# Optimization experiments

Measured on AMD Instinct MI355X. Metric: run time of the kernel, lower is better.

The kernel has to match this reference:

```python
import jax, jax.numpy as jnp
import numpy as np

B, S, H, I, E, TOP_K = 2, 2048, 1024, 2048, 8, 2


def setup_inputs() -> dict:
    key = jax.random.key(0)
    k1, k2, k3, k4, k5 = jax.random.split(key, 5)
    scale_h = 1.0 / np.sqrt(H)
    scale_i = 1.0 / np.sqrt(I)
    return {
        "hidden_states": jax.random.normal(k1, (B, S, H), dtype=jnp.float32),
        "router_w": jax.random.normal(k2, (H, E), dtype=jnp.float32) * scale_h,
        "gate_w": jax.random.normal(k3, (E, H, I), dtype=jnp.float32) * scale_h,
        "up_w": jax.random.normal(k4, (E, H, I), dtype=jnp.float32) * scale_h,
        "out_w": jax.random.normal(k5, (E, I, H), dtype=jnp.float32) * scale_i,
    }


def reference(hidden_states, router_w, gate_w, up_w, out_w):
    b, s, h = hidden_states.shape
    x = hidden_states.reshape(-1, h)  # [T, H], T = B*S

    # Router: logits -> softmax -> top-k -> renormalize -> dense routing matrix
    router_logits = x @ router_w  # [T, E]
    router_probs = jax.nn.softmax(router_logits, axis=-1)
    top_p, top_i = jax.lax.top_k(router_probs, TOP_K)  # [T, K]
    top_p = top_p / jnp.sum(top_p, axis=-1, keepdims=True)
    one_hot = jax.nn.one_hot(top_i, E, dtype=top_p.dtype)  # [T, K, E]
    routing_full = jnp.sum(one_hot * top_p[..., None], axis=1)  # [T, E]
    routing_full = routing_full.T  # [E, T]

    # Dense all-expert FFN (SwiGLU), as in the original batched einsum form
    gate = jnp.einsum("th,ehm->etm", x, gate_w)  # [E, T, I]
    gate = jax.nn.silu(gate)
    intermediate = jnp.einsum("th,ehm->etm", x, up_w)  # [E, T, I]
    hidden = intermediate * gate
    expert_out = jnp.einsum("eti,eih->eth", hidden, out_w)  # [E, T, H]

    # Weighted combine over experts
    out = jnp.sum(expert_out * routing_full[:, :, None], axis=0)  # [T, H]
    out = out.reshape(b, s, h)
    return out, router_logits
```

## Files before the change

### kernel.cpp

```cpp
#include <hip/hip_runtime.h>
#include <hip/hip_bf16.h>
#include <stdint.h>

#define TT 4096
#define HH 1024
#define II 2048
#define EE 8
#define RB 16
#define NRB (TT / RB)
#define CSTRIDE 32

typedef short bf16x8 __attribute__((ext_vector_type(8)));
typedef float f32x4 __attribute__((ext_vector_type(4)));

__device__ __forceinline__ unsigned short f2bf(float f) {
  unsigned u = __float_as_uint(f);
  u += 0x7FFF + ((u >> 16) & 1);
  return (unsigned short)(u >> 16);
}

__device__ __forceinline__ void gl_lds16(const void* g, void* l) {
  auto gp = reinterpret_cast<const __attribute__((address_space(1))) unsigned int*>(
      reinterpret_cast<uintptr_t>(g));
  auto lp = reinterpret_cast<__attribute__((address_space(3))) unsigned int*>(
      reinterpret_cast<uintptr_t>(l));
  __builtin_amdgcn_global_load_lds(gp, lp, 16, 0, 0);
}

__device__ __forceinline__ void transpose_tile_wide(const float* __restrict__ in,
                                                    unsigned short* __restrict__ out,
                                                    int M, int N, int mB, int nB,
                                                    unsigned int* tl, int tid) {
  union F4 { float4 v; float f[4]; };
  int n4 = tid & 31;
  int mph = tid >> 5;
  F4 a[4], bq[4];
  const float* base = in + (size_t)mB * N + nB + n4 * 4;
#pragma unroll
  for (int it = 0; it < 4; ++it) {
    const float* p = base + (size_t)(2 * (mph + it * 8)) * N;
    a[it].v = *(const float4*)p;
    bq[it].v = *(const float4*)(p + N);
  }
#pragma unroll
  for (int it = 0; it < 4; ++it) {
    int mp = mph + it * 8;
#pragma unroll
    for (int i = 0; i < 4; ++i) {
      int n = n4 * 4 + i;
      unsigned v = (unsigned)f2bf(a[it].f[i]) | ((unsigned)f2bf(bq[it].f[i]) << 16);
      tl[n * 32 + ((mp + (n >> 2) + (n & 3)) & 31)] = v;
    }
  }
  __syncthreads();
  int md = tid & 7;
  int nr = tid >> 3;
#pragma unroll
  for (int it = 0; it < 4; ++it) {
    int n = nr + it * 32;
    int rot = (n >> 2) + (n & 3);
    unsigned vv[4];
#pragma unroll
    for (int k = 0; k < 4; ++k)
      vv[k] = tl[n * 32 + ((md * 4 + k + rot) & 31)];
    *(uint4*)(out + (size_t)(nB + n) * M + mB + md * 8) = make_uint4(vv[0], vv[1], vv[2], vv[3]);
  }
}

__global__ __launch_bounds__(256, 4)
void front_kernel(const float* __restrict__ x, const float* __restrict__ rw,
                  const float* __restrict__ gw, const float* __restrict__ uw,
                  const float* __restrict__ ow,
                  float* __restrict__ logits_out, unsigned short* __restrict__ xb,
                  unsigned short* __restrict__ gwt, unsigned short* __restrict__ uwt,
                  unsigned short* __restrict__ owt,
                  int* __restrict__ gcnt, int2* __restrict__ ttop) {
  __shared__ unsigned int tl[4096];
  int b = blockIdx.x;
  int tid = threadIdx.x;

  if (b >= NRB) {
    int idx = b - NRB;
    int which = idx >> 11;
    int r = idx & 2047;
    int e = r >> 8;
    int tile = r & 255;
    if (which < 2) {
      int bx = tile & 15, by = tile >> 4;
      const float* in = (which ? uw : gw) + (size_t)e * HH * II;
      unsigned short* o = (which ? uwt : gwt) + (size_t)e * HH * II;
      transpose_tile_wide(in, o, HH, II, by * 64, bx * 128, tl, tid);
    } else {
      int bx = tile & 7, by = tile >> 3;
      transpose_tile_wide(ow + (size_t)e * II * HH, owt + (size_t)e * II * HH,
                          II, HH, by * 64, bx * 128, tl, tid);
    }
    return;
  }

  __shared__ int bcnt[EE];
  int wave = tid >> 6, lane = tid & 63;
  if (tid < EE) bcnt[tid] = 0;
  __syncthreads();
  int t0 = b * RB;

  for (int sub = 0; sub < RB / 4; ++sub) {
    int li = sub * 4 + wave;
    int t = t0 + li;
    float acc[EE];
#pragma unroll
    for (int e = 0; e < EE; ++e) acc[e] = 0.f;
#pragma unroll
    for (int j = 0; j < 4; ++j) {
      int h = j * 256 + lane * 4;
      union F4 { float4 v; float f[4]; } xv;
      xv.v = *(const float4*)(x + (size_t)t * HH + h);
      union { unsigned short s[4]; uint2 v; } pk;
#pragma unroll
      for (int i = 0; i < 4; ++i) pk.s[i] = f2bf(xv.f[i]);
      *(uint2*)(xb + (size_t)t * HH + h) = pk.v;
#pragma unroll
      for (int i = 0; i < 4; ++i) {
        const float4* r4 = (const float4*)(rw + (h + i) * EE);
        float4 r0 = r4[0], r1 = r4[1];
        float xs = xv.f[i];
        acc[0] += xs * r0.x; acc[1] += xs * r0.y; acc[2] += xs * r0.z; acc[3] += xs * r0.w;
        acc[4] += xs * r1.x; acc[5] += xs * r1.y; acc[6] += xs * r1.z; acc[7] += xs * r1.w;
      }
    }
#pragma unroll
    for (int e = 0; e < EE; ++e)
#pragma unroll
      for (int off = 32; off; off >>= 1) acc[e] += __shfl_down(acc[e], off);
    if (lane == 0) {
      float4* lo = (float4*)(logits_out + (size_t)t * EE);
      lo[0] = make_float4(acc[0], acc[1], acc[2], acc[3]);
      lo[1] = make_float4(acc[4], acc[5], acc[6], acc[7]);
      int e0 = 0; float b0 = acc[0];
#pragma unroll
      for (int e = 1; e < EE; ++e) if (acc[e] > b0) { b0 = acc[e]; e0 = e; }
      int e1 = -1; float b1 = -3.4e38f;
#pragma unroll
      for (int e = 0; e < EE; ++e) if (e != e0 && acc[e] > b1) { b1 = acc[e]; e1 = e; }
      float w0 = 1.f / (1.f + __expf(b1 - b0));
      int lp0 = atomicAdd(&bcnt[e0], 1);
      int lp1 = atomicAdd(&bcnt[e1], 1);
      ttop[t] = make_int2(e0 | (e1 << 3) | (lp0 << 6) | (lp1 << 11), __float_as_int(w0));
    }
  }
  __syncthreads();
  if (tid < EE) gcnt[b * EE + tid] = bcnt[tid];
}

__global__ void scatter_kernel(const int* __restrict__ gcnt, const int2* __restrict__ ttop,
                               int* __restrict__ cnt, int* __restrict__ list,
                               int* __restrict__ tslot, float2* __restrict__ tw) {
  __shared__ int raw[NRB * EE];
  __shared__ int base[NRB][EE];
  int tid = threadIdx.x;
  for (int i = tid; i < NRB * EE; i += 256) raw[i] = gcnt[i];
  __syncthreads();
  if (tid < EE) {
    int s = 0;
    for (int b = 0; b < NRB; ++b) { base[b][tid] = s; s += raw[b * EE + tid]; }
    if (blockIdx.x == 0) cnt[tid * CSTRIDE] = s;
  }
  __syncthreads();
  int t = blockIdx.x * 256 + tid;
  int2 ti = ttop[t];
  int v = ti.x;
  float w0 = __int_as_float(ti.y);
  int e0 = v & 7, e1 = (v >> 3) & 7, lp0 = (v >> 6) & 31, lp1 = (v >> 11) & 31;
  int b = t >> 4;
  int p0 = base[b][e0] + lp0;
  int p1 = base[b][e1] + lp1;
  list[e0 * TT + p0] = t;
  list[e1 * TT + p1] = t;
  tslot[t * 2]     = (e0 << 16) | p0;
  tslot[t * 2 + 1] = (e1 << 16) | p1;
  tw[t] = make_float2(w0, 1.f - w0);
}

__launch_bounds__(256, 3)
__global__ void gemm1_kernel(const unsigned short* __restrict__ xb,
                             const unsigned short* __restrict__ gwt,
                             const unsigned short* __restrict__ uwt,
                             unsigned short* __restrict__ hidden,
                             const int* __restrict__ cnt, const int* __restrict__ list) {
  __shared__ __align__(16) unsigned short smem[16384];
  __shared__ int stok[128];
  int tid = threadIdx.x;
  int e = blockIdx.z;

  int cn = cnt[e * CSTRIDE];
  int hb0 = 0;
  for (int i = 0; i < EE; ++i) hb0 += (i < e) ? cnt[i * CSTRIDE] : 0;
  int mBase = blockIdx.y * 128;
  if (mBase >= cn) return;
  int nBase = blockIdx.x * 64;

  int wave = tid >> 6, lane = tid & 63;
  if (tid < 128) {
    int g = mBase + tid;
    stok[tid] = list[e * TT + (g < cn ? g : cn - 1)];
  }
  __syncthreads();

  const char* gaddr[8];
#pragma unroll
  for (int j = 0; j < 8; ++j) {
    int c = wave * 512 + j * 64 + lane;
    const char* g;
    if (c < 1024) {
      int r = c >> 3, sl = (c & 7) ^ (r & 7);
      g = (const char*)xb + (size_t)stok[r] * (HH * 2) + sl * 16;
    } else if (c < 1536) {
      int cc = c - 1024, r = cc >> 3, sl = (cc & 7) ^ (r & 7);
      g = (const char*)gwt + ((size_t)e * II + nBase + r) * (HH * 2) + sl * 16;
    } else {
      int cc = c - 1536, r = cc >> 3, sl = (cc & 7) ^ (r & 7);
      g = (const char*)uwt + ((size_t)e * II + nBase + r) * (HH * 2) + sl * 16;
    }
    gaddr[j] = g;
  }

  int q = lane >> 4, m16 = lane & 15;
  int wr = wave & 1, wc = wave >> 1;
  int faddrA[4][2], faddrBg[2][2], faddrBu[2][2];
#pragma unroll
  for (int mi = 0; mi < 4; ++mi) {
    int R = wr * 64 + mi * 16 + m16;
#pragma unroll
    for (int h = 0; h < 2; ++h)
      faddrA[mi][h] = (R * 8 + ((h * 4 + q) ^ (R & 7))) * 16;
  }
#pragma unroll
  for (int ni = 0; ni < 2; ++ni) {
    int n = wc * 32 + ni * 16 + m16;
#pragma unroll
    for (int h = 0; h < 2; ++h) {
      faddrBg[ni][h] = (1024 + n * 8 + ((h * 4 + q) ^ (n & 7))) * 16;
      faddrBu[ni][h] = (1536 + n * 8 + ((h * 4 + q) ^ (n & 7))) * 16;
    }
  }

  f32x4 zero4 = {0.f, 0.f, 0.f, 0.f};
  f32x4 accG[4][2], accU[4][2];
#pragma unroll
  for (int mi = 0; mi < 4; ++mi)
#pragma unroll
    for (int ni = 0; ni < 2; ++ni) { accG[mi][ni] = zero4; accU[mi][ni] = zero4; }

  const char* smemc = (const char*)smem;
  for (int kt = 0; kt < HH / 64; ++kt) {
    __syncthreads();
#pragma unroll
    for (int j = 0; j < 8; ++j) {
      gl_lds16(gaddr[j], (char*)smem + (size_t)(wave * 512 + j * 64) * 16);
      gaddr[j] += 128;
    }
    __syncthreads();
#pragma unroll
    for (int h = 0; h < 2; ++h) {
      bf16x8 aF[4], bG[2], bU[2];
#pragma unroll
      for (int mi = 0; mi < 4; ++mi) aF[mi] = *(const bf16x8*)(smemc + faddrA[mi][h]);
#pragma unroll
      for (int ni = 0; ni < 2; ++ni) {
        bG[ni] = *(const bf16x8*)(smemc + faddrBg[ni][h]);
        bU[ni] = *(const bf16x8*)(smemc + faddrBu[ni][h]);
      }
#pragma unroll
      for (int mi = 0; mi < 4; ++mi)
#pragma unroll
        for (int ni = 0; ni < 2; ++ni) {
          accG[mi][ni] = __builtin_amdgcn_mfma_f32_16x16x32_bf16(aF[mi], bG[ni], accG[mi][ni], 0, 0, 0);
          accU[mi][ni] = __builtin_amdgcn_mfma_f32_16x16x32_bf16(aF[mi], bU[ni], accU[mi][ni], 0, 0, 0);
        }
    }
  }

  int hb = hb0 + mBase;
  int rowsValid = cn - mBase; if (rowsValid > 128) rowsValid = 128;
#pragma unroll
  for (int mi = 0; mi < 4; ++mi)
#pragma unroll
    for (int ni = 0; ni < 2; ++ni)
#pragma unroll
      for (int r = 0; r < 4; ++r) {
        int row = wr * 64 + mi * 16 + q * 4 + r;
        if (row < rowsValid) {
          float g = accG[mi][ni][r], u = accU[mi][ni][r];
          float h = g / (1.f + __expf(-g)) * u;
          hidden[(size_t)(hb + row) * II + nBase + wc * 32 + ni * 16 + m16] = f2bf(h);
        }
      }
}

__launch_bounds__(256, 3)
__global__ void gemm2_kernel(const unsigned short* __restrict__ hidden,
                             const unsigned short* __restrict__ owt,
                             float* __restrict__ expert_out,
                             const int* __restrict__ cnt) {
  int e = blockIdx.z;
  int cn = cnt[e * CSTRIDE];
  int hb0 = 0;
  for (int i = 0; i < EE; ++i) hb0 += (i < e) ? cnt[i * CSTRIDE] : 0;
  int mBase = blockIdx.y * 128;
  if (mBase >= cn) return;
  int nBase = blockIdx.x * 128;

  __shared__ __align__(16) unsigned short smem[16384];

  int tid = threadIdx.x, wave = tid >> 6, lane = tid & 63;
  int hb = hb0 + mBase;
  const char* gaddr[8];
#pragma unroll
  for (int j = 0; j < 8; ++j) {
    int c = wave * 512 + j * 64 + lane;
    const char* g;
    if (c < 1024) {
      int r = c >> 3, sl = (c & 7) ^ (r & 7);
      g = (const char*)hidden + (size_t)(hb + r) * (II * 2) + sl * 16;
    } else {
      int cc = c - 1024, r = cc >> 3, sl = (cc & 7) ^ (r & 7);
      g = (const char*)owt + ((size_t)e * HH + nBase + r) * (II * 2) + sl * 16;
    }
    gaddr[j] = g;
  }

  int q = lane >> 4, m16 = lane & 15;
  int wr = wave & 1, wc = wave >> 1;
  int faddrA[4][2], faddrB[4][2];
#pragma unroll
  for (int mi = 0; mi < 4; ++mi) {
    int R = wr * 64 + mi * 16 + m16;
#pragma unroll
    for (int h = 0; h < 2; ++h)
      faddrA[mi][h] = (R * 8 + ((h * 4 + q) ^ (R & 7))) * 16;
  }
#pragma unroll
  for (int ni = 0; ni < 4; ++ni) {
    int n = wc * 64 + ni * 16 + m16;
#pragma unroll
    for (int h = 0; h < 2; ++h)
      faddrB[ni][h] = (1024 + n * 8 + ((h * 4 + q) ^ (n & 7))) * 16;
  }

  f32x4 zero4 = {0.f, 0.f, 0.f, 0.f};
  f32x4 acc[4][4];
#pragma unroll
  for (int mi = 0; mi < 4; ++mi)
#pragma unroll
    for (int ni = 0; ni < 4; ++ni) acc[mi][ni] = zero4;

  const char* smemc = (const char*)smem;
  for (int kt = 0; kt < II / 64; ++kt) {
    __syncthreads();
#pragma unroll
    for (int j = 0; j < 8; ++j) {
      gl_lds16(gaddr[j], (char*)smem + (size_t)(wave * 512 + j * 64) * 16);
      gaddr[j] += 128;
    }
    __syncthreads();
#pragma unroll
    for (int h = 0; h < 2; ++h) {
      bf16x8 aF[4], bF[4];
#pragma unroll
      for (int mi = 0; mi < 4; ++mi) aF[mi] = *(const bf16x8*)(smemc + faddrA[mi][h]);
#pragma unroll
      for (int ni = 0; ni < 4; ++ni) bF[ni] = *(const bf16x8*)(smemc + faddrB[ni][h]);
#pragma unroll
      for (int mi = 0; mi < 4; ++mi)
#pragma unroll
        for (int ni = 0; ni < 4; ++ni)
          acc[mi][ni] = __builtin_amdgcn_mfma_f32_16x16x32_bf16(aF[mi], bF[ni], acc[mi][ni], 0, 0, 0);
    }
  }

  int rowsValid = cn - mBase; if (rowsValid > 128) rowsValid = 128;
#pragma unroll
  for (int mi = 0; mi < 4; ++mi)
#pragma unroll
    for (int ni = 0; ni < 4; ++ni)
#pragma unroll
      for (int r = 0; r < 4; ++r) {
        int row = wr * 64 + mi * 16 + q * 4 + r;
        if (row < rowsValid)
          expert_out[(size_t)(hb + row) * HH + nBase + wc * 64 + ni * 16 + m16] = acc[mi][ni][r];
      }
}

__global__ void combine_kernel(const float* __restrict__ expert_out,
                               const int* __restrict__ cnt, const int* __restrict__ tslot,
                               const float2* __restrict__ tw, float* __restrict__ out) {
  int pre[EE];
  int s = 0;
#pragma unroll
  for (int e = 0; e < EE; ++e) { pre[e] = s; s += cnt[e * CSTRIDE]; }
  int t = blockIdx.x;
  int s0 = tslot[t * 2], s1 = tslot[t * 2 + 1];
  float2 w = tw[t];
  int r0 = pre[s0 >> 16] + (s0 & 0xFFFF);
  int r1 = pre[s1 >> 16] + (s1 & 0xFFFF);
  const float4* a = (const float4*)(expert_out + (size_t)r0 * HH);
  const float4* b = (const float4*)(expert_out + (size_t)r1 * HH);
  float4* o = (float4*)(out + (size_t)t * HH);
  int c = threadIdx.x;
  float4 av = a[c], bv = b[c];
  o[c] = make_float4(w.x * av.x + w.y * bv.x, w.x * av.y + w.y * bv.y,
                     w.x * av.z + w.y * bv.z, w.x * av.w + w.y * bv.w);
}

extern "C" void kernel_launch(void* const* d_in, const int* in_sizes, int n_in,
                              void* d_out, int out_size, void* d_ws, size_t ws_size,
                              hipStream_t stream) {
  (void)in_sizes; (void)n_in; (void)out_size; (void)ws_size;
  const float* x  = (const float*)d_in[0];
  const float* rw = (const float*)d_in[1];
  const float* gw = (const float*)d_in[2];
  const float* uw = (const float*)d_in[3];
  const float* ow = (const float*)d_in[4];
  float* out = (float*)d_out;
  float* logits = out + (size_t)TT * HH;

  char* ws = (char*)d_ws;
  size_t o = 0;
  auto alloc = [&](size_t bytes) {
    char* p = ws + o;
    o += (bytes + 255) & ~(size_t)255;
    return p;
  };
  unsigned short* xb  = (unsigned short*)alloc((size_t)TT * HH * 2);
  unsigned short* gwt = (unsigned short*)alloc((size_t)EE * II * HH * 2);
  unsigned short* uwt = (unsigned short*)alloc((size_t)EE * II * HH * 2);
  unsigned short* owt = (unsigned short*)alloc((size_t)EE * HH * II * 2);
  unsigned short* hidden = (unsigned short*)alloc((size_t)(2 * TT + 128) * II * 2);
  int*    cnt   = (int*)alloc(EE * CSTRIDE * 4);
  int*    list  = (int*)alloc((size_t)EE * TT * 4);
  int*    tslot = (int*)alloc((size_t)TT * 2 * 4);
  float2* tw    = (float2*)alloc((size_t)TT * 8);
  int*    gcnt  = (int*)alloc((size_t)NRB * EE * 4);
  int2*   ttop  = (int2*)alloc((size_t)TT * 8);
  float* expert_out = (float*)gwt;

  front_kernel<<<NRB + 3 * 2048, 256, 0, stream>>>(x, rw, gw, uw, ow, logits, xb, gwt, uwt, owt,
                                                   gcnt, ttop);
  scatter_kernel<<<TT / 256, 256, 0, stream>>>(gcnt, ttop, cnt, list, tslot, tw);
  gemm1_kernel<<<dim3(32, 32, EE), 256, 0, stream>>>(xb, gwt, uwt, hidden, cnt, list);
  gemm2_kernel<<<dim3(HH / 128, TT / 128, EE), 256, 0, stream>>>(hidden, owt, expert_out, cnt);
  combine_kernel<<<TT, 256, 0, stream>>>(expert_out, cnt, tslot, tw, out);
}
```

Measured before the change: 398.9 us.

## Process four transpose tiles per block with double-buffered register prefetch

The weight transpose/convert path now handles four consecutive 64x128 tiles per block instead of one. The global loads for the next tile are issued into a second register set while the current tile is converted and written through an LDS buffer, alternating between two LDS buffers. The aim is to hide global load latency and amortize per-block launch overhead across tiles. In exchange, register use per thread and LDS per block both double, which may reduce occupancy in the shared front_kernel, including its router blocks.

After: 406.8 us. No clear change (+2.0%).

```diff
diff --git a/kernel.cpp b/kernel.cpp
--- a/kernel.cpp
+++ b/kernel.cpp
@@ -27,43 +27,56 @@
   __builtin_amdgcn_global_load_lds(gp, lp, 16, 0, 0);
 }
 
-__device__ __forceinline__ void transpose_tile_wide(const float* __restrict__ in,
-                                                    unsigned short* __restrict__ out,
-                                                    int M, int N, int mB, int nB,
-                                                    unsigned int* tl, int tid) {
+__device__ __forceinline__ void transpose_quad(const float* __restrict__ in,
+                                               unsigned short* __restrict__ out,
+                                               int M, int N, int mB, int bx0,
+                                               unsigned int* tl, int tid) {
   union F4 { float4 v; float f[4]; };
   int n4 = tid & 31;
   int mph = tid >> 5;
-  F4 a[4], bq[4];
-  const float* base = in + (size_t)mB * N + nB + n4 * 4;
-#pragma unroll
-  for (int it = 0; it < 4; ++it) {
-    const float* p = base + (size_t)(2 * (mph + it * 8)) * N;
-    a[it].v = *(const float4*)p;
-    bq[it].v = *(const float4*)(p + N);
-  }
-#pragma unroll
-  for (int it = 0; it < 4; ++it) {
-    int mp = mph + it * 8;
-#pragma unroll
-    for (int i = 0; i < 4; ++i) {
-      int n = n4 * 4 + i;
-      unsigned v = (unsigned)f2bf(a[it].f[i]) | ((unsigned)f2bf(bq[it].f[i]) << 16);
-      tl[n * 32 + ((mp + (n >> 2) + (n & 3)) & 31)] = v;
-    }
-  }
-  __syncthreads();
-  int md = tid & 7;
-  int nr = tid >> 3;
-#pragma unroll
-  for (int it = 0; it < 4; ++it) {
-    int n = nr + it * 32;
-    int rot = (n >> 2) + (n & 3);
-    unsigned vv[4];
-#pragma unroll
-    for (int k = 0; k < 4; ++k)
-      vv[k] = tl[n * 32 + ((md * 4 + k + rot) & 31)];
-    *(uint4*)(out + (size_t)(nB + n) * M + mB + md * 8) = make_uint4(vv[0], vv[1], vv[2], vv[3]);
+  F4 R0[8], R1[8];
+
+  auto issue = [&](F4* R, int nB) {
+    const float* base = in + (size_t)(mB + 2 * mph) * N + nB + n4 * 4;
+#pragma unroll
+    for (int it = 0; it < 4; ++it) {
+      const float* p = base + (size_t)(2 * it * 8) * N;
+      R[it].v = *(const float4*)p;
+      R[4 + it].v = *(const float4*)(p + N);
+    }
+  };
+
+  issue(R0, bx0 * 128);
+#pragma unroll
+  for (int i = 0; i < 4; ++i) {
+    F4* cur = (i & 1) ? R1 : R0;
+    F4* nxt = (i & 1) ? R0 : R1;
+    if (i < 3) issue(nxt, (bx0 + i + 1) * 128);
+    unsigned int* buf = tl + (i & 1) * 4096;
+    int nB = (bx0 + i) * 128;
+#pragma unroll
+    for (int it = 0; it < 4; ++it) {
+      int mp = mph + it * 8;
+#pragma unroll
+      for (int k = 0; k < 4; ++k) {
+        int n = n4 * 4 + k;
+        unsigned v = (unsigned)f2bf(cur[it].f[k]) | ((unsigned)f2bf(cur[4 + it].f[k]) << 16);
+        buf[n * 32 + ((mp + (n >> 2) + (n & 3)) & 31)] = v;
+      }
+    }
+    __syncthreads();
+    int md = tid & 7;
+    int nr = tid >> 3;
+#pragma unroll
+    for (int it = 0; it < 4; ++it) {
+      int n = nr + it * 32;
+      int rot = (n >> 2) + (n & 3);
+      unsigned vv[4];
+#pragma unroll
+      for (int k = 0; k < 4; ++k)
+        vv[k] = buf[n * 32 + ((md * 4 + k + rot) & 31)];
+      *(uint4*)(out + (size_t)(nB + n) * M + mB + md * 8) = make_uint4(vv[0], vv[1], vv[2], vv[3]);
+    }
   }
 }
 
@@ -75,25 +88,25 @@
                   unsigned short* __restrict__ gwt, unsigned short* __restrict__ uwt,
                   unsigned short* __restrict__ owt,
                   int* __restrict__ gcnt, int2* __restrict__ ttop) {
-  __shared__ unsigned int tl[4096];
+  __shared__ unsigned int tl[8192];
   int b = blockIdx.x;
   int tid = threadIdx.x;
 
   if (b >= NRB) {
     int idx = b - NRB;
-    int which = idx >> 11;
-    int r = idx & 2047;
-    int e = r >> 8;
-    int tile = r & 255;
+    int which = idx >> 9;
+    int r = idx & 511;
+    int e = r >> 6;
+    int blk = r & 63;
     if (which < 2) {
-      int bx = tile & 15, by = tile >> 4;
+      int mB = (blk >> 2) * 64, bx0 = (blk & 3) * 4;
       const float* in = (which ? uw : gw) + (size_t)e * HH * II;
       unsigned short* o = (which ? uwt : gwt) + (size_t)e * HH * II;
-      transpose_tile_wide(in, o, HH, II, by * 64, bx * 128, tl, tid);
+      transpose_quad(in, o, HH, II, mB, bx0, tl, tid);
     } else {
-      int bx = tile & 7, by = tile >> 3;
-      transpose_tile_wide(ow + (size_t)e * II * HH, owt + (size_t)e * II * HH,
-                          II, HH, by * 64, bx * 128, tl, tid);
+      int mB = (blk >> 1) * 64, bx0 = (blk & 1) * 4;
+      transpose_quad(ow + (size_t)e * II * HH, owt + (size_t)e * II * HH,
+                     II, HH, mB, bx0, tl, tid);
     }
     return;
   }
@@ -444,8 +457,8 @@
   int2*   ttop  = (int2*)alloc((size_t)TT * 8);
   float* expert_out = (float*)gwt;
 
-  front_kernel<<<NRB + 3 * 2048, 256, 0, stream>>>(x, rw, gw, uw, ow, logits, xb, gwt, uwt, owt,
-                                                   gcnt, ttop);
+  front_kernel<<<NRB + 3 * 512, 256, 0, stream>>>(x, rw, gw, uw, ow, logits, xb, gwt, uwt, owt,
+                                                  gcnt, ttop);
   scatter_kernel<<<TT / 256, 256, 0, stream>>>(gcnt, ttop, cnt, list, tslot, tw);
   gemm1_kernel<<<dim3(32, 32, EE), 256, 0, stream>>>(xb, gwt, uwt, hidden, cnt, list);
   gemm2_kernel<<<dim3(HH / 128, TT / 128, EE), 256, 0, stream>>>(hidden, owt, expert_out, cnt);
```

## Double-buffer LDS tiles with K=32 steps in both expert GEMMs

Applied to the files above, without the earlier changes.

Both expert GEMM kernels now split their 32KB of LDS into two 16KB buffers with a K-tile of 32 instead of one 32KB buffer with a K-tile of 64. The direct global-to-LDS loads for the next tile are issued before the MFMA work on the current tile, leaving one barrier per iteration. The aim is to hide global load latency behind matrix math instead of stalling on a load-then-compute barrier pair. To match the new 4-chunk row width, the XOR swizzle changes to (row>>1)&3. Each tile now feeds half as many MFMAs, so per-iteration overhead is relatively larger.

After: 419.3 us. +5.1%, slower.

```diff
diff --git a/kernel.cpp b/kernel.cpp
--- a/kernel.cpp
+++ b/kernel.cpp
@@ -206,42 +206,39 @@
   }
   __syncthreads();
 
-  const char* gaddr[8];
-#pragma unroll
-  for (int j = 0; j < 8; ++j) {
-    int c = wave * 512 + j * 64 + lane;
+  const char* gaddr[4];
+  int lofs[4];
+#pragma unroll
+  for (int j = 0; j < 4; ++j) {
+    int c = wave * 256 + j * 64 + lane;
     const char* g;
-    if (c < 1024) {
-      int r = c >> 3, sl = (c & 7) ^ (r & 7);
-      g = (const char*)xb + (size_t)stok[r] * (HH * 2) + sl * 16;
-    } else if (c < 1536) {
-      int cc = c - 1024, r = cc >> 3, sl = (cc & 7) ^ (r & 7);
-      g = (const char*)gwt + ((size_t)e * II + nBase + r) * (HH * 2) + sl * 16;
+    if (c < 512) {
+      int r = c >> 2, kc = (c & 3) ^ ((r >> 1) & 3);
+      g = (const char*)xb + (size_t)stok[r] * (HH * 2) + kc * 16;
+    } else if (c < 768) {
+      int cc = c - 512, r = cc >> 2, kc = (cc & 3) ^ ((r >> 1) & 3);
+      g = (const char*)gwt + ((size_t)e * II + nBase + r) * (HH * 2) + kc * 16;
     } else {
-      int cc = c - 1536, r = cc >> 3, sl = (cc & 7) ^ (r & 7);
-      g = (const char*)uwt + ((size_t)e * II + nBase + r) * (HH * 2) + sl * 16;
+      int cc = c - 768, r = cc >> 2, kc = (cc & 3) ^ ((r >> 1) & 3);
+      g = (const char*)uwt + ((size_t)e * II + nBase + r) * (HH * 2) + kc * 16;
     }
     gaddr[j] = g;
+    lofs[j] = c * 16;
   }
 
   int q = lane >> 4, m16 = lane & 15;
   int wr = wave & 1, wc = wave >> 1;
-  int faddrA[4][2], faddrBg[2][2], faddrBu[2][2];
+  int faddrA[4], faddrBg[2], faddrBu[2];
 #pragma unroll
   for (int mi = 0; mi < 4; ++mi) {
     int R = wr * 64 + mi * 16 + m16;
-#pragma unroll
-    for (int h = 0; h < 2; ++h)
-      faddrA[mi][h] = (R * 8 + ((h * 4 + q) ^ (R & 7))) * 16;
+    faddrA[mi] = (R * 4 + (q ^ ((R >> 1) & 3))) * 16;
   }
 #pragma unroll
   for (int ni = 0; ni < 2; ++ni) {
     int n = wc * 32 + ni * 16 + m16;
-#pragma unroll
-    for (int h = 0; h < 2; ++h) {
-      faddrBg[ni][h] = (1024 + n * 8 + ((h * 4 + q) ^ (n & 7))) * 16;
-      faddrBu[ni][h] = (1536 + n * 8 + ((h * 4 + q) ^ (n & 7))) * 16;
-    }
+    faddrBg[ni] = (512 + n * 4 + (q ^ ((n >> 1) & 3))) * 16;
+    faddrBu[ni] = (768 + n * 4 + (q ^ ((n >> 1) & 3))) * 16;
   }
 
   f32x4 zero4 = {0.f, 0.f, 0.f, 0.f};
@@ -251,33 +248,41 @@
 #pragma unroll
     for (int ni = 0; ni < 2; ++ni) { accG[mi][ni] = zero4; accU[mi][ni] = zero4; }
 
-  const char* smemc = (const char*)smem;
-  for (int kt = 0; kt < HH / 64; ++kt) {
+  char* smemc = (char*)smem;
+#pragma unroll
+  for (int j = 0; j < 4; ++j) {
+    gl_lds16(gaddr[j], smemc + lofs[j]);
+    gaddr[j] += 64;
+  }
+  __syncthreads();
+
+  const int NK = HH / 32;
+  for (int kt = 0; kt < NK; ++kt) {
+    int cur = kt & 1;
+    if (kt + 1 < NK) {
+#pragma unroll
+      for (int j = 0; j < 4; ++j) {
+        gl_lds16(gaddr[j], smemc + (cur ^ 1) * 16384 + lofs[j]);
+        gaddr[j] += 64;
+      }
+    }
+    const char* sb = smemc + cur * 16384;
+    bf16x8 aF[4], bG[2], bU[2];
+#pragma unroll
+    for (int mi = 0; mi < 4; ++mi) aF[mi] = *(const bf16x8*)(sb + faddrA[mi]);
+#pragma unroll
+    for (int ni = 0; ni < 2; ++ni) {
+      bG[ni] = *(const bf16x8*)(sb + faddrBg[ni]);
+      bU[ni] = *(const bf16x8*)(sb + faddrBu[ni]);
+    }
+#pragma unroll
+    for (int mi = 0; mi < 4; ++mi)
+#pragma unroll
+      for (int ni = 0; ni < 2; ++ni) {
+        accG[mi][ni] = __builtin_amdgcn_mfma_f32_16x16x32_bf16(aF[mi], bG[ni], accG[mi][ni], 0, 0, 0);
+        accU[mi][ni] = __builtin_amdgcn_mfma_f32_16x16x32_bf16(aF[mi], bU[ni], accU[mi][ni], 0, 0, 0);
+      }
     __syncthreads();
-#pragma unroll
-    for (int j = 0; j < 8; ++j) {
-      gl_lds16(gaddr[j], (char*)smem + (size_t)(wave * 512 + j * 64) * 16);
-      gaddr[j] += 128;
-    }
-    __syncthreads();
-#pragma unroll
-    for (int h = 0; h < 2; ++h) {
-      bf16x8 aF[4], bG[2], bU[2];
-#pragma unroll
-      for (int mi = 0; mi < 4; ++mi) aF[mi] = *(const bf16x8*)(smemc + faddrA[mi][h]);
-#pragma unroll
-      for (int ni = 0; ni < 2; ++ni) {
-        bG[ni] = *(const bf16x8*)(smemc + faddrBg[ni][h]);
-        bU[ni] = *(const bf16x8*)(smemc + faddrBu[ni][h]);
-      }
-#pragma unroll
-      for (int mi = 0; mi < 4; ++mi)
-#pragma unroll
-        for (int ni = 0; ni < 2; ++ni) {
-          accG[mi][ni] = __builtin_amdgcn_mfma_f32_16x16x32_bf16(aF[mi], bG[ni], accG[mi][ni], 0, 0, 0);
-          accU[mi][ni] = __builtin_amdgcn_mfma_f32_16x16x32_bf16(aF[mi], bU[ni], accU[mi][ni], 0, 0, 0);
-        }
-    }
   }
 
   int hb = hb0 + mBase;
@@ -314,37 +319,35 @@
 
   int tid = threadIdx.x, wave = tid >> 6, lane = tid & 63;
   int hb = hb0 + mBase;
-  const char* gaddr[8];
-#pragma unroll
-  for (int j = 0; j < 8; ++j) {
-    int c = wave * 512 + j * 64 + lane;
+  const char* gaddr[4];
+  int lofs[4];
+#pragma unroll
+  for (int j = 0; j < 4; ++j) {
+    int c = wave * 256 + j * 64 + lane;
     const char* g;
-    if (c < 1024) {
-      int r = c >> 3, sl = (c & 7) ^ (r & 7);
-      g = (const char*)hidden + (size_t)(hb + r) * (II * 2) + sl * 16;
+    if (c < 512) {
+      int r = c >> 2, kc = (c & 3) ^ ((r >> 1) & 3);
+      g = (const char*)hidden + (size_t)(hb + r) * (II * 2) + kc * 16;
     } else {
-      int cc = c - 1024, r = cc >> 3, sl = (cc & 7) ^ (r & 7);
-      g = (const char*)owt + ((size_t)e * HH + nBase + r) * (II * 2) + sl * 16;
+      int cc = c - 512, r = cc >> 2, kc = (cc & 3) ^ ((r >> 1) & 3);
+      g = (const char*)owt + ((size_t)e * HH + nBase + r) * (II * 2) + kc * 16;
     }
     gaddr[j] = g;
+    lofs[j] = c * 16;
   }
 
   int q = lane >> 4, m16 = lane & 15;
   int wr = wave & 1, wc = wave >> 1;
-  int faddrA[4][2], faddrB[4][2];
+  int faddrA[4], faddrB[4];
 #pragma unroll
   for (int mi = 0; mi < 4; ++mi) {
     int R = wr * 64 + mi * 16 + m16;
-#pragma unroll
-    for (int h = 0; h < 2; ++h)
-      faddrA[mi][h] = (R * 8 + ((h * 4 + q) ^ (R & 7))) * 16;
+    faddrA[mi] = (R * 4 + (q ^ ((R >> 1) & 3))) * 16;
   }
 #pragma unroll
   for (int ni = 0; ni < 4; ++ni) {
     int n = wc * 64 + ni * 16 + m16;
-#pragma unroll
-    for (int h = 0; h < 2; ++h)
-      faddrB[ni][h] = (1024 + n * 8 + ((h * 4 + q) ^ (n & 7))) * 16;
+    faddrB[ni] = (512 + n * 4 + (q ^ ((n >> 1) & 3))) * 16;
   }
 
   f32x4 zero4 = {0.f, 0.f, 0.f, 0.f};
@@ -354,28 +357,36 @@
 #pragma unroll
     for (int ni = 0; ni < 4; ++ni) acc[mi][ni] = zero4;
 
-  const char* smemc = (const char*)smem;
-  for (int kt = 0; kt < II / 64; ++kt) {
+  char* smemc = (char*)smem;
+#pragma unroll
+  for (int j = 0; j < 4; ++j) {
+    gl_lds16(gaddr[j], smemc + lofs[j]);
+    gaddr[j] += 64;
+  }
+  __syncthreads();
+
+  const int NK = II / 32;
+  for (int kt = 0; kt < NK; ++kt) {
+    int cur = kt & 1;
+    if (kt + 1 < NK) {
+#pragma unroll
+      for (int j = 0; j < 4; ++j) {
+        gl_lds16(gaddr[j], smemc + (cur ^ 1) * 16384 + lofs[j]);
+        gaddr[j] += 64;
+      }
+    }
+    const char* sb = smemc + cur * 16384;
+    bf16x8 aF[4], bF[4];
+#pragma unroll
+    for (int mi = 0; mi < 4; ++mi) aF[mi] = *(const bf16x8*)(sb + faddrA[mi]);
+#pragma unroll
+    for (int ni = 0; ni < 4; ++ni) bF[ni] = *(const bf16x8*)(sb + faddrB[ni]);
+#pragma unroll
+    for (int mi = 0; mi < 4; ++mi)
+#pragma unroll
+      for (int ni = 0; ni < 4; ++ni)
+        acc[mi][ni] = __builtin_amdgcn_mfma_f32_16x16x32_bf16(aF[mi], bF[ni], acc[mi][ni], 0, 0, 0);
     __syncthreads();
-#pragma unroll
-    for (int j = 0; j < 8; ++j) {
-      gl_lds16(gaddr[j], (char*)smem + (size_t)(wave * 512 + j * 64) * 16);
-      gaddr[j] += 128;
-    }
-    __syncthreads();
-#pragma unroll
-    for (int h = 0; h < 2; ++h) {
-      bf16x8 aF[4], bF[4];
-#pragma unroll
-      for (int mi = 0; mi < 4; ++mi) aF[mi] = *(const bf16x8*)(smemc + faddrA[mi][h]);
-#pragma unroll
-      for (int ni = 0; ni < 4; ++ni) bF[ni] = *(const bf16x8*)(smemc + faddrB[ni][h]);
-#pragma unroll
-      for (int mi = 0; mi < 4; ++mi)
-#pragma unroll
-        for (int ni = 0; ni < 4; ++ni)
-          acc[mi][ni] = __builtin_amdgcn_mfma_f32_16x16x32_bf16(aF[mi], bF[ni], acc[mi][ni], 0, 0, 0);
-    }
   }
 
   int rowsValid = cn - mBase; if (rowsValid > 128) rowsValid = 128;
```

## Fuse weighted combine into gemm2 via atomics and move out_w transpose into gemm1

Applied to the files above, without the earlier changes.

Drops the separate combine kernel and the fp32 expert_out buffer. gemm2 now scales each output row by its routing weight and atomically adds it into the zero-initialised output, and the output is zeroed by extra blocks in the front kernel. The out_w transpose moves from the front kernel into extra blocks of gemm1, so it can overlap with the first GEMM. The cost is float atomics on global memory, which make the summation order nondeterministic, and more blocks in the gemm1 launch.

After: 398.3 us. Within noise of the previous version (-0.1%).

```diff
diff --git a/kernel.cpp b/kernel.cpp
--- a/kernel.cpp
+++ b/kernel.cpp
@@ -9,6 +9,8 @@
 #define RB 16
 #define NRB (TT / RB)
 #define CSTRIDE 32
+#define NTRB (2 * 2048)
+#define NZB 256
 
 typedef short bf16x8 __attribute__((ext_vector_type(8)));
 typedef float f32x4 __attribute__((ext_vector_type(4)));
@@ -70,14 +72,22 @@
 __global__ __launch_bounds__(256, 4)
 void front_kernel(const float* __restrict__ x, const float* __restrict__ rw,
                   const float* __restrict__ gw, const float* __restrict__ uw,
-                  const float* __restrict__ ow,
                   float* __restrict__ logits_out, unsigned short* __restrict__ xb,
                   unsigned short* __restrict__ gwt, unsigned short* __restrict__ uwt,
-                  unsigned short* __restrict__ owt,
-                  int* __restrict__ gcnt, int2* __restrict__ ttop) {
+                  int* __restrict__ gcnt, int2* __restrict__ ttop,
+                  float* __restrict__ outz) {
   __shared__ unsigned int tl[4096];
   int b = blockIdx.x;
   int tid = threadIdx.x;
+
+  if (b >= NRB + NTRB) {
+    int zb = b - NRB - NTRB;
+    float4* o = (float4*)outz + (size_t)zb * 4096 + tid;
+    float4 z = make_float4(0.f, 0.f, 0.f, 0.f);
+#pragma unroll
+    for (int k = 0; k < 16; ++k) o[k * 256] = z;
+    return;
+  }
 
   if (b >= NRB) {
     int idx = b - NRB;
@@ -85,16 +95,10 @@
     int r = idx & 2047;
     int e = r >> 8;
     int tile = r & 255;
-    if (which < 2) {
-      int bx = tile & 15, by = tile >> 4;
-      const float* in = (which ? uw : gw) + (size_t)e * HH * II;
-      unsigned short* o = (which ? uwt : gwt) + (size_t)e * HH * II;
-      transpose_tile_wide(in, o, HH, II, by * 64, bx * 128, tl, tid);
-    } else {
-      int bx = tile & 7, by = tile >> 3;
-      transpose_tile_wide(ow + (size_t)e * II * HH, owt + (size_t)e * II * HH,
-                          II, HH, by * 64, bx * 128, tl, tid);
-    }
+    int bx = tile & 15, by = tile >> 4;
+    const float* in = (which ? uw : gw) + (size_t)e * HH * II;
+    unsigned short* o = (which ? uwt : gwt) + (size_t)e * HH * II;
+    transpose_tile_wide(in, o, HH, II, by * 64, bx * 128, tl, tid);
     return;
   }
 
@@ -154,7 +158,7 @@
 
 __global__ void scatter_kernel(const int* __restrict__ gcnt, const int2* __restrict__ ttop,
                                int* __restrict__ cnt, int* __restrict__ list,
-                               int* __restrict__ tslot, float2* __restrict__ tw) {
+                               float* __restrict__ rwt) {
   __shared__ int raw[NRB * EE];
   __shared__ int base[NRB][EE];
   int tid = threadIdx.x;
@@ -176,21 +180,29 @@
   int p1 = base[b][e1] + lp1;
   list[e0 * TT + p0] = t;
   list[e1 * TT + p1] = t;
-  tslot[t * 2]     = (e0 << 16) | p0;
-  tslot[t * 2 + 1] = (e1 << 16) | p1;
-  tw[t] = make_float2(w0, 1.f - w0);
+  rwt[e0 * TT + p0] = w0;
+  rwt[e1 * TT + p1] = 1.f - w0;
 }
 
 __launch_bounds__(256, 3)
 __global__ void gemm1_kernel(const unsigned short* __restrict__ xb,
                              const unsigned short* __restrict__ gwt,
                              const unsigned short* __restrict__ uwt,
+                             const float* __restrict__ ow, unsigned short* __restrict__ owt,
                              unsigned short* __restrict__ hidden,
                              const int* __restrict__ cnt, const int* __restrict__ list) {
   __shared__ __align__(16) unsigned short smem[16384];
   __shared__ int stok[128];
   int tid = threadIdx.x;
   int e = blockIdx.z;
+
+  if (blockIdx.y >= 32) {
+    int tile = (blockIdx.y - 32) * 32 + blockIdx.x;
+    int bx = tile & 7, by = tile >> 3;
+    transpose_tile_wide(ow + (size_t)e * II * HH, owt + (size_t)e * II * HH,
+                        II, HH, by * 64, bx * 128, (unsigned int*)smem, tid);
+    return;
+  }
 
   int cn = cnt[e * CSTRIDE];
   int hb0 = 0;
@@ -300,8 +312,9 @@
 __launch_bounds__(256, 3)
 __global__ void gemm2_kernel(const unsigned short* __restrict__ hidden,
                              const unsigned short* __restrict__ owt,
-                             float* __restrict__ expert_out,
-                             const int* __restrict__ cnt) {
+                             float* __restrict__ out,
+                             const int* __restrict__ cnt, const int* __restrict__ list,
+                             const float* __restrict__ rwt) {
   int e = blockIdx.z;
   int cn = cnt[e * CSTRIDE];
   int hb0 = 0;
@@ -311,9 +324,18 @@
   int nBase = blockIdx.x * 128;
 
   __shared__ __align__(16) unsigned short smem[16384];
+  __shared__ int stok[128];
+  __shared__ float swt[128];
 
   int tid = threadIdx.x, wave = tid >> 6, lane = tid & 63;
   int hb = hb0 + mBase;
+  if (tid < 128) {
+    int g = mBase + tid;
+    int gi = g < cn ? g : cn - 1;
+    stok[tid] = list[e * TT + gi];
+    swt[tid] = rwt[e * TT + gi];
+  }
+
   const char* gaddr[8];
 #pragma unroll
   for (int j = 0; j < 8; ++j) {
@@ -382,34 +404,17 @@
 #pragma unroll
   for (int mi = 0; mi < 4; ++mi)
 #pragma unroll
-    for (int ni = 0; ni < 4; ++ni)
-#pragma unroll
-      for (int r = 0; r < 4; ++r) {
-        int row = wr * 64 + mi * 16 + q * 4 + r;
-        if (row < rowsValid)
-          expert_out[(size_t)(hb + row) * HH + nBase + wc * 64 + ni * 16 + m16] = acc[mi][ni][r];
+    for (int r = 0; r < 4; ++r) {
+      int row = wr * 64 + mi * 16 + q * 4 + r;
+      if (row < rowsValid) {
+        int t = stok[row];
+        float w = swt[row];
+        float* orow = out + (size_t)t * HH + nBase + wc * 64 + m16;
+#pragma unroll
+        for (int ni = 0; ni < 4; ++ni)
+          atomicAdd(orow + ni * 16, w * acc[mi][ni][r]);
       }
-}
-
-__global__ void combine_kernel(const float* __restrict__ expert_out,
-                               const int* __restrict__ cnt, const int* __restrict__ tslot,
-                               const float2* __restrict__ tw, float* __restrict__ out) {
-  int pre[EE];
-  int s = 0;
-#pragma unroll
-  for (int e = 0; e < EE; ++e) { pre[e] = s; s += cnt[e * CSTRIDE]; }
-  int t = blockIdx.x;
-  int s0 = tslot[t * 2], s1 = tslot[t * 2 + 1];
-  float2 w = tw[t];
-  int r0 = pre[s0 >> 16] + (s0 & 0xFFFF);
-  int r1 = pre[s1 >> 16] + (s1 & 0xFFFF);
-  const float4* a = (const float4*)(expert_out + (size_t)r0 * HH);
-  const float4* b = (const float4*)(expert_out + (size_t)r1 * HH);
-  float4* o = (float4*)(out + (size_t)t * HH);
-  int c = threadIdx.x;
-  float4 av = a[c], bv = b[c];
-  o[c] = make_float4(w.x * av.x + w.y * bv.x, w.x * av.y + w.y * bv.y,
-                     w.x * av.z + w.y * bv.z, w.x * av.w + w.y * bv.w);
+    }
 }
 
 extern "C" void kernel_launch(void* const* d_in, const int* in_sizes, int n_in,
@@ -438,16 +443,13 @@
   unsigned short* hidden = (unsigned short*)alloc((size_t)(2 * TT + 128) * II * 2);
   int*    cnt   = (int*)alloc(EE * CSTRIDE * 4);
   int*    list  = (int*)alloc((size_t)EE * TT * 4);
-  int*    tslot = (int*)alloc((size_t)TT * 2 * 4);
-  float2* tw    = (float2*)alloc((size_t)TT * 8);
+  float*  rwt   = (float*)alloc((size_t)EE * TT * 4);
   int*    gcnt  = (int*)alloc((size_t)NRB * EE * 4);
   int2*   ttop  = (int2*)alloc((size_t)TT * 8);
-  float* expert_out = (float*)gwt;
-
-  front_kernel<<<NRB + 3 * 2048, 256, 0, stream>>>(x, rw, gw, uw, ow, logits, xb, gwt, uwt, owt,
-                                                   gcnt, ttop);
-  scatter_kernel<<<TT / 256, 256, 0, stream>>>(gcnt, ttop, cnt, list, tslot, tw);
-  gemm1_kernel<<<dim3(32, 32, EE), 256, 0, stream>>>(xb, gwt, uwt, hidden, cnt, list);
-  gemm2_kernel<<<dim3(HH / 128, TT / 128, EE), 256, 0, stream>>>(hidden, owt, expert_out, cnt);
-  combine_kernel<<<TT, 256, 0, stream>>>(expert_out, cnt, tslot, tw, out);
-}
+
+  front_kernel<<<NRB + NTRB + NZB, 256, 0, stream>>>(x, rw, gw, uw, logits, xb, gwt, uwt,
+                                                     gcnt, ttop, out);
+  scatter_kernel<<<TT / 256, 256, 0, stream>>>(gcnt, ttop, cnt, list, rwt);
+  gemm1_kernel<<<dim3(32, 40, EE), 256, 0, stream>>>(xb, gwt, uwt, ow, owt, hidden, cnt, list);
+  gemm2_kernel<<<dim3(HH / 128, TT / 128, EE), 256, 0, stream>>>(hidden, owt, out, cnt, list, rwt);
+}
```
